# Kernel optimization log

Measured on AMD Instinct MI355X. Metric: run time of the kernel, lower is better.

The kernel has to match this reference:

```python
import jax, jax.numpy as jnp
import numpy as np

B, N, H, W = 8, 128, 128, 128


def setup_inputs() -> dict:
    key = jax.random.key(0)
    k1, k2, k3 = jax.random.split(key, 3)
    logit = jax.random.normal(k1, (B, N, H, W), dtype=jnp.float32)
    target = jax.random.randint(k2, (B, H, W), 0, N, dtype=jnp.int64)
    weight = jax.random.uniform(k3, (B, N), dtype=jnp.float32)
    return {"logit": logit, "target": target, "weight": weight, "epoch": 1}


def reference(logit, target, weight, epoch):
    # Seesaw loss (weight branch). p = 1, C = ones, reduction = 'mean'.
    exp = jnp.exp(logit)  # [B, N, H, W]
    # Mitigation matrix M[b, i, j] = (w_i / w_j)**p if w_i > w_j else 1
    wi = weight[:, :, None]  # [B, N, 1]
    wj = weight[:, None, :]  # [B, 1, N]
    M = jnp.where(wi > wj, wi / wj, jnp.float32(1.0))  # [B, N, N]
    # numerator: exp at the target class per pixel -> [B, H, W]
    num = jnp.take_along_axis(exp, target[:, None, :, :], axis=1)[:, 0]
    # tmp_c[b, j, h, w] = sum_i exp[b, i, h, w] * M[b, i, j]  (C is all ones)
    denom = jnp.einsum("bihw,bij->bjhw", exp, M)  # [B, N, H, W]
    denom_t = jnp.take_along_axis(denom, target[:, None, :, :], axis=1)[:, 0]
    log = -jnp.log(num / denom_t)  # [B, H, W]
    return log.mean()
```

## Files before the change

### kernel.cpp

```cpp
#include <hip/hip_runtime.h>


#define B_    8
#define N_    128
#define HALF_N 64
#define HW_   16384
#define NPIX  (B_ * HW_)
#define BLOCK 256
#define PIX_PER_BLOCK 128
#define BLOCKS_PER_B  (HW_ / PIX_PER_BLOCK)
#define NBLOCKS (B_ * BLOCKS_PER_B)

__global__ __launch_bounds__(BLOCK) void seesaw_main(
    const float* __restrict__ logit,
    const int*   __restrict__ target,
    const float* __restrict__ weight,
    float*       __restrict__ partials)
{
    __shared__ float w_s[N_];
    __shared__ float sa[PIX_PER_BLOCK];
    __shared__ float sl[PIX_PER_BLOCK];
    __shared__ float red[BLOCK / 64];

    const int b    = blockIdx.x >> 7;
    const int pl   = threadIdx.x & 127;
    const int half = threadIdx.x >> 7;
    const int pix  = (blockIdx.x & 127) * PIX_PER_BLOCK + pl;

    if (threadIdx.x < N_) w_s[threadIdx.x] = weight[b * N_ + threadIdx.x];
    __syncthreads();

    const int   t  = target[b * HW_ + pix];
    const float wt = w_s[t];

    const float* lp = logit + (size_t)b * N_ * HW_ + (size_t)half * HALF_N * HW_ + pix;
    const int ibase = half * HALF_N;

    float a  = 0.0f;
    float lt = 0.0f;

    #pragma unroll 16
    for (int k = 0; k < HALF_N; ++k) {
        const float l  = lp[(size_t)k * HW_];
        const float wi = w_s[ibase + k];
        a  = fmaf(__expf(l), fmaxf(wi, wt), a);
        lt = (ibase + k == t) ? l : lt;
    }

    if (half) { sa[pl] = a; sl[pl] = lt; }
    __syncthreads();

    float loss = 0.0f;
    if (!half) {
        const float at = a + sa[pl];
        const float lf = lt + sl[pl];
        loss = __logf(at) - __logf(wt) - lf;
    }

    #pragma unroll
    for (int o = 32; o > 0; o >>= 1) loss += __shfl_down(loss, o, 64);

    const int lane = threadIdx.x & 63;
    const int wid  = threadIdx.x >> 6;
    if (lane == 0) red[wid] = loss;
    __syncthreads();

    if (threadIdx.x == 0) {
        float s = 0.0f;
        #pragma unroll
        for (int k = 0; k < BLOCK / 64; ++k) s += red[k];
        partials[blockIdx.x] = s;
    }
}

__global__ __launch_bounds__(1024) void seesaw_reduce(
    const float* __restrict__ partials,
    float*       __restrict__ out)
{
    __shared__ float red[16];
    float s = partials[threadIdx.x];

    #pragma unroll
    for (int o = 32; o > 0; o >>= 1) s += __shfl_down(s, o, 64);

    const int lane = threadIdx.x & 63;
    const int wid  = threadIdx.x >> 6;
    if (lane == 0) red[wid] = s;
    __syncthreads();

    if (threadIdx.x == 0) {
        float tot = 0.0f;
        #pragma unroll
        for (int k = 0; k < 16; ++k) tot += red[k];
        out[0] = tot * (1.0f / (float)NPIX);
    }
}

extern "C" void kernel_launch(void* const* d_in, const int* in_sizes, int n_in,
                              void* d_out, int out_size, void* d_ws, size_t ws_size,
                              hipStream_t stream)
{
    const float* logit  = (const float*)d_in[0];
    const int*   target = (const int*)  d_in[1];
    const float* weight = (const float*)d_in[2];

    float* partials = (float*)d_ws;
    float* out      = (float*)d_out;

    seesaw_main<<<NBLOCKS, BLOCK, 0, stream>>>(logit, target, weight, partials);
    seesaw_reduce<<<1, 1024, 0, stream>>>(partials, out);
}
```

Before: 18.40 us.

## Split classes across eight waves per block and fuse final reduction via atomics

```diff
diff --git a/kernel.cpp b/kernel.cpp
--- a/kernel.cpp
+++ b/kernel.cpp
@@ -3,29 +3,32 @@
 
 #define B_    8
 #define N_    128
-#define HALF_N 64
 #define HW_   16384
 #define NPIX  (B_ * HW_)
-#define BLOCK 256
-#define PIX_PER_BLOCK 128
-#define BLOCKS_PER_B  (HW_ / PIX_PER_BLOCK)
+#define BLOCK 512
+#define OCTS  8
+#define E_    16
+#define PX    64
+#define BLOCKS_PER_B (HW_ / PX)
 #define NBLOCKS (B_ * BLOCKS_PER_B)
 
-__global__ __launch_bounds__(BLOCK) void seesaw_main(
+__global__ __launch_bounds__(BLOCK, 8) void seesaw_main(
     const float* __restrict__ logit,
     const int*   __restrict__ target,
     const float* __restrict__ weight,
-    float*       __restrict__ partials)
+    float*       __restrict__ acc,
+    unsigned int* __restrict__ cnt,
+    float*       __restrict__ out)
 {
     __shared__ float w_s[N_];
-    __shared__ float sa[PIX_PER_BLOCK];
-    __shared__ float sl[PIX_PER_BLOCK];
-    __shared__ float red[BLOCK / 64];
+    __shared__ float sa[OCTS][PX];
+    __shared__ float sl[OCTS][PX];
 
-    const int b    = blockIdx.x >> 7;
-    const int pl   = threadIdx.x & 127;
-    const int half = threadIdx.x >> 7;
-    const int pix  = (blockIdx.x & 127) * PIX_PER_BLOCK + pl;
+    const int b    = blockIdx.x >> 8;
+    const int pix0 = (blockIdx.x & 255) * PX;
+    const int pl   = threadIdx.x & 63;
+    const int oct  = threadIdx.x >> 6;
+    const int pix  = pix0 + pl;
 
     if (threadIdx.x < N_) w_s[threadIdx.x] = weight[b * N_ + threadIdx.x];
     __syncthreads();
@@ -33,66 +36,43 @@
     const int   t  = target[b * HW_ + pix];
     const float wt = w_s[t];
 
-    const float* lp = logit + (size_t)b * N_ * HW_ + (size_t)half * HALF_N * HW_ + pix;
-    const int ibase = half * HALF_N;
+    const int ibase = oct * E_;
+    const float* lp = logit + (size_t)(b * N_ + ibase) * HW_ + pix;
 
     float a  = 0.0f;
     float lt = 0.0f;
 
-    #pragma unroll 16
-    for (int k = 0; k < HALF_N; ++k) {
+    #pragma unroll 8
+    for (int k = 0; k < E_; ++k) {
         const float l  = lp[(size_t)k * HW_];
         const float wi = w_s[ibase + k];
         a  = fmaf(__expf(l), fmaxf(wi, wt), a);
         lt = (ibase + k == t) ? l : lt;
     }
 
-    if (half) { sa[pl] = a; sl[pl] = lt; }
+    sa[oct][pl] = a;
+    sl[oct][pl] = lt;
     __syncthreads();
 
     float loss = 0.0f;
-    if (!half) {
-        const float at = a + sa[pl];
-        const float lf = lt + sl[pl];
+    if (oct == 0) {
+        float at = 0.0f, lf = 0.0f;
+        #pragma unroll
+        for (int k = 0; k < OCTS; ++k) { at += sa[k][pl]; lf += sl[k][pl]; }
         loss = __logf(at) - __logf(wt) - lf;
+
+        #pragma unroll
+        for (int o = 32; o > 0; o >>= 1) loss += __shfl_down(loss, o, 64);
     }
 
-    #pragma unroll
-    for (int o = 32; o > 0; o >>= 1) loss += __shfl_down(loss, o, 64);
-
-    const int lane = threadIdx.x & 63;
-    const int wid  = threadIdx.x >> 6;
-    if (lane == 0) red[wid] = loss;
-    __syncthreads();
-
     if (threadIdx.x == 0) {
-        float s = 0.0f;
-        #pragma unroll
-        for (int k = 0; k < BLOCK / 64; ++k) s += red[k];
-        partials[blockIdx.x] = s;
-    }
-}
-
-__global__ __launch_bounds__(1024) void seesaw_reduce(
-    const float* __restrict__ partials,
-    float*       __restrict__ out)
-{
-    __shared__ float red[16];
-    float s = partials[threadIdx.x];
-
-    #pragma unroll
-    for (int o = 32; o > 0; o >>= 1) s += __shfl_down(s, o, 64);
-
-    const int lane = threadIdx.x & 63;
-    const int wid  = threadIdx.x >> 6;
-    if (lane == 0) red[wid] = s;
-    __syncthreads();
-
-    if (threadIdx.x == 0) {
-        float tot = 0.0f;
-        #pragma unroll
-        for (int k = 0; k < 16; ++k) tot += red[k];
-        out[0] = tot * (1.0f / (float)NPIX);
+        atomicAdd(acc, loss);
+        __threadfence();
+        const unsigned int old = atomicAdd(cnt, 1u);
+        if (old == NBLOCKS - 1) {
+            const float total = atomicAdd(acc, 0.0f);
+            out[0] = total * (1.0f / (float)NPIX);
+        }
     }
 }
 
@@ -104,9 +84,10 @@
     const int*   target = (const int*)  d_in[1];
     const float* weight = (const float*)d_in[2];
 
-    float* partials = (float*)d_ws;
-    float* out      = (float*)d_out;
+    float*        acc = (float*)d_ws;
+    unsigned int* cnt = (unsigned int*)((char*)d_ws + sizeof(float));
+    float*        out = (float*)d_out;
 
-    seesaw_main<<<NBLOCKS, BLOCK, 0, stream>>>(logit, target, weight, partials);
-    seesaw_reduce<<<1, 1024, 0, stream>>>(partials, out);
+    hipMemsetAsync(d_ws, 0, 2 * sizeof(float), stream);
+    seesaw_main<<<NBLOCKS, BLOCK, 0, stream>>>(logit, target, weight, acc, cnt, out);
 }
```

Measured after the change: 72.79 us. 296% more time.

## Split class dimension into eight slices with float2 pixel loads per thread

Applied to the files above, without the earlier changes.

```diff
diff --git a/kernel.cpp b/kernel.cpp
--- a/kernel.cpp
+++ b/kernel.cpp
@@ -3,12 +3,13 @@
 
 #define B_    8
 #define N_    128
-#define HALF_N 64
 #define HW_   16384
 #define NPIX  (B_ * HW_)
 #define BLOCK 256
-#define PIX_PER_BLOCK 128
-#define BLOCKS_PER_B  (HW_ / PIX_PER_BLOCK)
+#define PX    64
+#define OCTS  8
+#define CPT   16
+#define BLOCKS_PER_B (HW_ / PX)
 #define NBLOCKS (B_ * BLOCKS_PER_B)
 
 __global__ __launch_bounds__(BLOCK) void seesaw_main(
@@ -18,59 +19,55 @@
     float*       __restrict__ partials)
 {
     __shared__ float w_s[N_];
-    __shared__ float sa[PIX_PER_BLOCK];
-    __shared__ float sl[PIX_PER_BLOCK];
-    __shared__ float red[BLOCK / 64];
+    __shared__ float sa[OCTS][PX];
+    __shared__ int   t_s[PX];
 
-    const int b    = blockIdx.x >> 7;
-    const int pl   = threadIdx.x & 127;
-    const int half = threadIdx.x >> 7;
-    const int pix  = (blockIdx.x & 127) * PIX_PER_BLOCK + pl;
+    const int b    = blockIdx.x >> 8;
+    const int pix0 = (blockIdx.x & 255) * PX;
+    const int pp   = threadIdx.x & 31;
+    const int q    = threadIdx.x >> 5;
+    const int px   = pp * 2;
 
     if (threadIdx.x < N_) w_s[threadIdx.x] = weight[b * N_ + threadIdx.x];
     __syncthreads();
 
-    const int   t  = target[b * HW_ + pix];
-    const float wt = w_s[t];
+    const int2 t2 = *(const int2*)(target + b * HW_ + pix0 + px);
+    if (q == 0) *(int2*)&t_s[px] = t2;
 
-    const float* lp = logit + (size_t)b * N_ * HW_ + (size_t)half * HALF_N * HW_ + pix;
-    const int ibase = half * HALF_N;
+    const float wt0 = w_s[t2.x];
+    const float wt1 = w_s[t2.y];
 
-    float a  = 0.0f;
-    float lt = 0.0f;
+    const int ibase = q * CPT;
+    const float* lp = logit + (size_t)(b * N_ + ibase) * HW_ + pix0 + px;
 
-    #pragma unroll 16
-    for (int k = 0; k < HALF_N; ++k) {
-        const float l  = lp[(size_t)k * HW_];
+    float a0 = 0.0f, a1 = 0.0f;
+
+    #pragma unroll
+    for (int k = 0; k < CPT; ++k) {
+        const float2 l = *(const float2*)(lp + (size_t)k * HW_);
         const float wi = w_s[ibase + k];
-        a  = fmaf(__expf(l), fmaxf(wi, wt), a);
-        lt = (ibase + k == t) ? l : lt;
+        a0 = fmaf(__expf(l.x), fmaxf(wi, wt0), a0);
+        a1 = fmaf(__expf(l.y), fmaxf(wi, wt1), a1);
     }
 
-    if (half) { sa[pl] = a; sl[pl] = lt; }
+    *(float2*)&sa[q][px] = make_float2(a0, a1);
     __syncthreads();
 
     float loss = 0.0f;
-    if (!half) {
-        const float at = a + sa[pl];
-        const float lf = lt + sl[pl];
-        loss = __logf(at) - __logf(wt) - lf;
+    if (threadIdx.x < PX) {
+        const int p = threadIdx.x;
+        float at = 0.0f;
+        #pragma unroll
+        for (int k = 0; k < OCTS; ++k) at += sa[k][p];
+        const int   t  = t_s[p];
+        const float wt = w_s[t];
+        const float lt = logit[(size_t)(b * N_ + t) * HW_ + pix0 + p];
+        loss = __logf(at) - __logf(wt) - lt;
+
+        #pragma unroll
+        for (int o = 32; o > 0; o >>= 1) loss += __shfl_down(loss, o, 64);
     }
-
-    #pragma unroll
-    for (int o = 32; o > 0; o >>= 1) loss += __shfl_down(loss, o, 64);
-
-    const int lane = threadIdx.x & 63;
-    const int wid  = threadIdx.x >> 6;
-    if (lane == 0) red[wid] = loss;
-    __syncthreads();
-
-    if (threadIdx.x == 0) {
-        float s = 0.0f;
-        #pragma unroll
-        for (int k = 0; k < BLOCK / 64; ++k) s += red[k];
-        partials[blockIdx.x] = s;
-    }
+    if (threadIdx.x == 0) partials[blockIdx.x] = loss;
 }
 
 __global__ __launch_bounds__(1024) void seesaw_reduce(
@@ -78,7 +75,7 @@
     float*       __restrict__ out)
 {
     __shared__ float red[16];
-    float s = partials[threadIdx.x];
+    float s = partials[threadIdx.x] + partials[threadIdx.x + 1024];
 
     #pragma unroll
     for (int o = 32; o > 0; o >>= 1) s += __shfl_down(s, o, 64);
```

Measured after the change: 18.29 us. About the same (-0.6%).
